# Performance work log

Hardware: AMD Instinct MI355X
Metric: run time of the kernel (lower is better)

Reference implementation:

```python
import jax, jax.numpy as jnp
import numpy as np

ALPHA = 0.2
N_ENT, N_TYP, N_REL, E = 100000, 1000, 200, 500000
D = 64          # nfeat1 = nfeat2 = nhid1 = nhid2 = relation_dim
NHEADS = 2      # forced by the tuple-unpack in the original forward


def _xavier(key, shape):
    fan_out, fan_in = shape[0], shape[-1]
    lim = 1.414 * np.sqrt(6.0 / (fan_in + fan_out))
    return jax.random.uniform(key, shape, jnp.float32, -lim, lim)


def setup_inputs() -> dict:
    key = jax.random.key(0)
    ks = jax.random.split(key, 32)
    inp = {
        "entity_embeddings": jax.random.normal(ks[0], (N_ENT, D), jnp.float32),
        "type_embed": jax.random.normal(ks[1], (N_TYP, D), jnp.float32),
        "relation_embed": jax.random.normal(ks[2], (N_REL, D), jnp.float32),
        "edge_list": jax.random.randint(ks[3], (2, E), 0, N_TYP),  # row0=src entity, row1=dst type; both in-range
        "edge_type": jax.random.randint(ks[4], (E,), 0, N_REL),
        "edge_embed": jax.random.normal(ks[5], (E, D), jnp.float32),
    }
    Din = 3 * D  # cat(x1[src], x2[dst], edge_embed)
    i = 6
    for h in range(NHEADS):
        inp[f"a_e{h}"] = _xavier(ks[i], (D, Din)); i += 1   # entity-side attention proj
        inp[f"v_e{h}"] = _xavier(ks[i], (1, D))[0]; i += 1  # entity-side score vector
        inp[f"a_t{h}"] = _xavier(ks[i], (D, Din)); i += 1   # type-side attention proj
        inp[f"v_t{h}"] = _xavier(ks[i], (1, D))[0]; i += 1
    Ho = NHEADS * D       # 128
    Dout = 3 * Ho         # out layer input cat dim
    inp["a_eo"] = _xavier(ks[i], (Ho, Dout)); i += 1
    inp["v_eo"] = _xavier(ks[i], (1, Ho))[0]; i += 1
    inp["a_to"] = _xavier(ks[i], (Ho, Dout)); i += 1
    inp["v_to"] = _xavier(ks[i], (1, Ho))[0]; i += 1
    inp["W"] = _xavier(ks[i], (D, Ho))  # relation_dim -> nheads*nhid1
    return inp


def _gat_e2t(x1, x2, src, dst, e, a_e, v_e, a_t, v_t, concat):
    """Bipartite sparse GAT layer (KBGAT-style, e2t variant).
    Message m = a @ cat(x1[src], x2[dst], edge_embed); score = exp(-leaky_relu(v . m));
    softmax-normalized scatter-aggregate to entity nodes (by src) and type nodes (by dst)."""
    d1, d2 = x1.shape[1], x2.shape[1]

    def agg(a, v, seg, nseg):
        a1, a2, a3 = a[:, :d1], a[:, d1:d1 + d2], a[:, d1 + d2:]
        # project nodes first, then gather (avoids materializing [E, 3d] cat)
        m = (x1 @ a1.T)[src] + (x2 @ a2.T)[dst] + e @ a3.T     # [E, h]
        s = jnp.exp(-jax.nn.leaky_relu(m @ v, ALPHA))          # [E] unnormalized attention
        num = jax.ops.segment_sum(m * s[:, None], seg, num_segments=nseg)
        den = jax.ops.segment_sum(s, seg, num_segments=nseg)
        h = num / jnp.where(den == 0, 1.0, den)[:, None]
        return jax.nn.elu(h) if concat else h

    h_e = agg(a_e, v_e, src, x1.shape[0])
    h_t = agg(a_t, v_t, dst, x2.shape[0])
    return h_e, h_t


def reference(entity_embeddings, type_embed, relation_embed, edge_list, edge_type, edge_embed,
              a_e0, v_e0, a_t0, v_t0, a_e1, v_e1, a_t1, v_t1,
              a_eo, v_eo, a_to, v_to, W):
    src, dst = edge_list[0], edge_list[1]
    # two attention heads (concat=True -> elu inside)
    h0e, h0t = _gat_e2t(entity_embeddings, type_embed, src, dst, edge_embed, a_e0, v_e0, a_t0, v_t0, True)
    h1e, h1t = _gat_e2t(entity_embeddings, type_embed, src, dst, edge_embed, a_e1, v_e1, a_t1, v_t1, True)
    x1 = jnp.concatenate([h0e, h1e], axis=1)  # [N_ENT, 2*nhid1]
    x2 = jnp.concatenate([h0t, h1t], axis=1)  # [N_TYP, 2*nhid2]
    # dropout is identity at inference
    out_rel = relation_embed @ W              # [N_REL, nheads*nhid1]
    e2 = out_rel[edge_type]                   # per-edge relation embedding
    o1, o2 = _gat_e2t(x1, x2, src, dst, e2, a_eo, v_eo, a_to, v_to, False)
    return jax.nn.elu(o1), jax.nn.elu(o2), out_rel
```

## Files before the change

kernel.cpp:

```cpp
#include <hip/hip_runtime.h>

#define ALPHA 0.2f
#define NT 1000
#define NRELC 200
#define NE 500000
#define N_ENT 100000
#define CH 2048
#define G 245

static constexpr size_t I_STARTS_SRC = 0;
static constexpr size_t I_STARTS_DST = 1001;
static constexpr size_t I_COLSUM     = 2002;
static constexpr size_t I_HIST2      = 4002;
static constexpr size_t I_BASE2      = 494002;
static constexpr size_t I_AB_SRC     = 984004;
static constexpr size_t I_AB_DST     = 2984004;

static constexpr size_t F_U1 = 4984004;
static constexpr size_t F_U2 = F_U1 + 768;
static constexpr size_t F_L1 = F_U2 + 768;
static constexpr size_t F_X1 = F_L1 + 4*130000;
static constexpr size_t F_X2 = F_X1 + 128000;
static constexpr size_t F_OR = F_X2 + 128000;
static constexpr size_t F_L2 = F_OR + 25600;
static constexpr size_t S2F = 283800;
static constexpr size_t WS_FLOATS = F_L2 + 2*S2F;

static constexpr size_t OUT_O2  = 12800000;
static constexpr size_t OUT_REL = 12928000;

__device__ __forceinline__ float eluf(float x) { return x > 0.f ? x : expm1f(x); }
__device__ __forceinline__ float scoref(float slin) {
  return expf(slin > 0.f ? -slin : -ALPHA * slin);
}

__global__ __launch_bounds__(256) void k_hist2(const int* __restrict__ src,
                                               const int* __restrict__ dst,
                                               int* __restrict__ ip) {
  __shared__ int h[NT];
  int bid = blockIdx.x;
  int side = bid >= G;
  int blk = bid - side * G;
  const int* keys = side ? dst : src;
  int j0 = blk * CH;
  int n = min(CH, NE - j0);
  for (int i = threadIdx.x; i < NT; i += 256) h[i] = 0;
  __syncthreads();
  for (int k = threadIdx.x; k < n; k += 256) atomicAdd(&h[keys[j0 + k]], 1);
  __syncthreads();
  int* row = ip + I_HIST2 + (size_t)(side * G + blk) * NT;
  for (int b = threadIdx.x; b < NT; b += 256) row[b] = h[b];
}

__global__ void k_colsum(int* __restrict__ ip) {
  int t = blockIdx.x * 256 + threadIdx.x;
  if (t >= 2 * NT) return;
  int side = t / NT, bin = t - side * NT;
  int s = 0;
  for (int blk = 0; blk < G; ++blk)
    s += ip[I_HIST2 + (size_t)(side * G + blk) * NT + bin];
  ip[I_COLSUM + t] = s;
}

__global__ void k_scan2b(int* __restrict__ ip) {
  __shared__ int buf[1024];
  int t = threadIdx.x;
  for (int side = 0; side < 2; ++side) {
    int v = (t < NT) ? ip[I_COLSUM + side * NT + t] : 0;
    buf[t] = v;
    __syncthreads();
    for (int off = 1; off < 1024; off <<= 1) {
      int x = (t >= off) ? buf[t - off] : 0;
      __syncthreads();
      buf[t] += x;
      __syncthreads();
    }
    int* st = ip + (side ? I_STARTS_DST : I_STARTS_SRC);
    if (t < NT) st[t] = buf[t] - v;
    if (t == NT - 1) st[NT] = buf[t];
    __syncthreads();
  }
}

__global__ void k_bases(int* __restrict__ ip) {
  int t = blockIdx.x * 256 + threadIdx.x;
  if (t >= 2 * NT) return;
  int side = t / NT, bin = t - side * NT;
  int run = ip[(side ? I_STARTS_DST : I_STARTS_SRC) + bin];
  for (int blk = 0; blk < G; ++blk) {
    size_t idx = I_HIST2 + (size_t)(side * G + blk) * NT + bin;
    int c = ip[idx];
    ip[idx + (I_BASE2 - I_HIST2)] = run;
    run += c;
  }
}

__global__ void k_prep_u(const float* aE0, const float* vE0, const float* aT0, const float* vT0,
                         const float* aE1, const float* vE1, const float* aT1, const float* vT1,
                         const float* aEo, const float* vEo, const float* aTo, const float* vTo,
                         float* ws) {
  int t = blockIdx.x * blockDim.x + threadIdx.x;
  if (t < 768) {
    int c = t / 192, rem = t - c*192;
    int p = rem >> 6, k = rem & 63;
    const float* a = (c==0)?aE0:(c==1)?aT0:(c==2)?aE1:aT1;
    const float* v = (c==0)?vE0:(c==1)?vT0:(c==2)?vE1:vT1;
    float s = 0.f;
    for (int o = 0; o < 64; ++o) s += a[o*192 + p*64 + k] * v[o];
    ws[F_U1 + (size_t)(c*3+p)*64 + k] = s;
  } else if (t < 1536) {
    int tt = t - 768;
    int c = tt / 384, rem = tt - c*384;
    int p = rem >> 7, k = rem & 127;
    const float* a = c ? aTo : aEo;
    const float* v = c ? vTo : vEo;
    float s = 0.f;
    for (int o = 0; o < 128; ++o) s += a[o*384 + p*128 + k] * v[o];
    ws[F_U2 + (size_t)(c*3+p)*128 + k] = s;
  }
}

__global__ __launch_bounds__(256) void k_l1_proj(const float* Ent, const float* Typ,
                                                 const float* aE0, const float* aT0,
                                                 const float* aE1, const float* aT1,
                                                 float* ws) {
  int bid = blockIdx.x;
  int t = threadIdx.x;
  if (bid < 504) {
    __shared__ float xs[16][64];
    int c = bid / 126, rem = bid - c*126;
    int table = rem / 63, tile = rem - table*63;
    int i0 = tile * 16;
    const float* a = (c==0)?aE0:(c==1)?aT0:(c==2)?aE1:aT1;
    const float* x = table ? Typ : Ent;
    float* outb = ws + F_L1 + (size_t)c*130000 + (table ? 64000 : 0);
    for (int idx = t; idx < 1024; idx += 256) {
      int r = idx >> 6, k = idx & 63;
      int i = i0 + r;
      xs[r][k] = (i < NT) ? x[(size_t)i*64 + k] : 0.f;
    }
    __syncthreads();
    int o = t & 63, grp = t >> 6;
    const float* arow = a + o*192 + table*64;
    float acc0 = 0.f, acc1 = 0.f, acc2 = 0.f, acc3 = 0.f;
    #pragma unroll 8
    for (int k = 0; k < 64; ++k) {
      float av = arow[k];
      acc0 += xs[grp*4+0][k] * av;
      acc1 += xs[grp*4+1][k] * av;
      acc2 += xs[grp*4+2][k] * av;
      acc3 += xs[grp*4+3][k] * av;
    }
    int ib = i0 + grp*4;
    if (ib + 0 < NT) outb[(size_t)(ib+0)*64 + o] = acc0;
    if (ib + 1 < NT) outb[(size_t)(ib+1)*64 + o] = acc1;
    if (ib + 2 < NT) outb[(size_t)(ib+2)*64 + o] = acc2;
    if (ib + 3 < NT) outb[(size_t)(ib+3)*64 + o] = acc3;
  } else {
    int idx = (bid - 504) * 256 + t;
    if (idx >= 8000) return;
    int c = idx / 2000, rem = idx - c*2000;
    float* base = ws + F_L1 + (size_t)c * 130000;
    if (rem < 1000) {
      const float* x = Ent + (size_t)rem*64;
      const float* u = ws + F_U1 + (size_t)(c*3)*64;
      float s = 0.f;
      #pragma unroll
      for (int k = 0; k < 64; ++k) s += x[k]*u[k];
      base[128000 + rem] = s;
    } else {
      int i = rem - 1000;
      const float* x = Typ + (size_t)i*64;
      const float* u = ws + F_U1 + (size_t)(c*3+1)*64;
      float s = 0.f;
      #pragma unroll
      for (int k = 0; k < 64; ++k) s += x[k]*u[k];
      base[129000 + i] = s;
    }
  }
}

__global__ __launch_bounds__(256) void k_binscat(const int* __restrict__ src,
                                                 const int* __restrict__ dst,
                                                 const int* __restrict__ et,
                                                 int* __restrict__ ip,
                                                 const float* __restrict__ ws) {
  __shared__ int2 bufs[CH];
  __shared__ int loff[1024];
  __shared__ int lcur[1024];
  __shared__ int gbase[1024];
  __shared__ int psum[256];
  int bid = blockIdx.x;
  int side = bid >= G;
  int blk = bid - side * G;
  const int* keys = side ? dst : src;
  const int* oths = side ? src : dst;
  int j0 = blk * CH;
  int n = min(CH, NE - j0);
  int t = threadIdx.x;

  for (int i = t; i < 1024; i += 256) lcur[i] = 0;
  __syncthreads();
  for (int k = t; k < n; k += 256) atomicAdd(&lcur[keys[j0 + k]], 1);
  __syncthreads();
  int c0 = lcur[4*t], c1 = lcur[4*t+1], c2 = lcur[4*t+2], c3 = lcur[4*t+3];
  int s = c0 + c1 + c2 + c3;
  psum[t] = s;
  __syncthreads();
  for (int off = 1; off < 256; off <<= 1) {
    int x = (t >= off) ? psum[t - off] : 0;
    __syncthreads();
    psum[t] += x;
    __syncthreads();
  }
  int base = psum[t] - s;
  loff[4*t]   = base;
  loff[4*t+1] = base + c0;
  loff[4*t+2] = base + c0 + c1;
  loff[4*t+3] = base + c0 + c1 + c2;
  lcur[4*t]   = loff[4*t];
  lcur[4*t+1] = loff[4*t+1];
  lcur[4*t+2] = loff[4*t+2];
  lcur[4*t+3] = loff[4*t+3];
  const int* brow = ip + I_BASE2 + (size_t)(side * G + blk) * NT;
  for (int b = t; b < NT; b += 256) gbase[b] = brow[b];
  __syncthreads();
  for (int k = t; k < n; k += 256) {
    int j = j0 + k;
    int b = keys[j];
    int pos = atomicAdd(&lcur[b], 1);
    bufs[pos] = make_int2(j | (b << 19), oths[j] | (et[j] << 16));
  }
  __syncthreads();
  size_t othOff = side ? 128000 : 129000;
  const float* cT0 = ws + F_L1 + (size_t)(side    )*130000 + othOff;
  const float* cT1 = ws + F_L1 + (size_t)(side + 2)*130000 + othOff;
  int4* out4 = reinterpret_cast<int4*>(ip + (side ? I_AB_DST : I_AB_SRC));
  for (int k = t; k < n; k += 256) {
    int2 q = bufs[k];
    int b = q.x >> 19;
    int posg = gbase[b] + (k - loff[b]);
    int oth = q.y & 0xFFFF;
    out4[posg] = make_int4(q.x & 0x7FFFF, q.y,
                           __float_as_int(cT0[oth]), __float_as_int(cT1[oth]));
  }
}

__global__ __launch_bounds__(256) void k_l1_acc(const float* __restrict__ Eemb,
                                                const float* aE0, const float* aT0,
                                                const float* aE1, const float* aT1,
                                                const int* __restrict__ ip,
                                                float* __restrict__ ws) {
  __shared__ float smem[3154];
  float* TlB   = smem;
  float* accRf = smem + 2000;
  float* accEf = smem + 3024;
  float* denf  = smem + 3152;
  float* redf  = smem + 2000;

  int side = blockIdx.x >= NT;
  int g = blockIdx.x - side * NT;
  int t = threadIdx.x;
  int sub = t & 15, slot = t >> 4;
  int c0 = side, c1 = side + 2;

  size_t ownOff = side ? 129000 : 128000;
  for (int i = t; i < NT; i += 256) { TlB[i] = 0.f; TlB[1000 + i] = 0.f; }
  if (t < 2) denf[t] = 0.f;
  float ownA = ws[F_L1 + (size_t)c0*130000 + ownOff + g];
  float ownB = ws[F_L1 + (size_t)c1*130000 + ownOff + g];
  float4 w3A = reinterpret_cast<const float4*>(ws + F_U1 + (size_t)(c0*3+2)*64)[sub];
  float4 w3B = reinterpret_cast<const float4*>(ws + F_U1 + (size_t)(c1*3+2)*64)[sub];
  __syncthreads();

  int start = ip[(side ? I_STARTS_DST : I_STARTS_SRC) + g];
  int end   = ip[(side ? I_STARTS_DST : I_STARTS_SRC) + g + 1];
  const int4* ab = reinterpret_cast<const int4*>(ip + (side ? I_AB_DST : I_AB_SRC));
  const float4* EV = reinterpret_cast<const float4*>(Eemb);

  float4 acc0 = make_float4(0.f,0.f,0.f,0.f);
  float4 acc1 = make_float4(0.f,0.f,0.f,0.f);
  float d0 = 0.f, d1 = 0.f;

  int p = start + slot;
  for (; p + 48 < end; p += 64) {
    int4 q0 = ab[p], q1 = ab[p+16], q2 = ab[p+32], q3 = ab[p+48];
    float4 e0 = EV[(size_t)q0.x*16 + sub];
    float4 e1 = EV[(size_t)q1.x*16 + sub];
    float4 e2 = EV[(size_t)q2.x*16 + sub];
    float4 e3 = EV[(size_t)q3.x*16 + sub];
    float rA0 = e0.x*w3A.x + e0.y*w3A.y + e0.z*w3A.z + e0.w*w3A.w;
    float rB0 = e0.x*w3B.x + e0.y*w3B.y + e0.z*w3B.z + e0.w*w3B.w;
    float rA1 = e1.x*w3A.x + e1.y*w3A.y + e1.z*w3A.z + e1.w*w3A.w;
    float rB1 = e1.x*w3B.x + e1.y*w3B.y + e1.z*w3B.z + e1.w*w3B.w;
    float rA2 = e2.x*w3A.x + e2.y*w3A.y + e2.z*w3A.z + e2.w*w3A.w;
    float rB2 = e2.x*w3B.x + e2.y*w3B.y + e2.z*w3B.z + e2.w*w3B.w;
    float rA3 = e3.x*w3A.x + e3.y*w3A.y + e3.z*w3A.z + e3.w*w3A.w;
    float rB3 = e3.x*w3B.x + e3.y*w3B.y + e3.z*w3B.z + e3.w*w3B.w;
    #pragma unroll
    for (int sh = 1; sh < 16; sh <<= 1) {
      rA0 += __shfl_xor(rA0, sh, 16); rB0 += __shfl_xor(rB0, sh, 16);
      rA1 += __shfl_xor(rA1, sh, 16); rB1 += __shfl_xor(rB1, sh, 16);
      rA2 += __shfl_xor(rA2, sh, 16); rB2 += __shfl_xor(rB2, sh, 16);
      rA3 += __shfl_xor(rA3, sh, 16); rB3 += __shfl_xor(rB3, sh, 16);
    }
    int o0 = q0.y & 0xFFFF, o1 = q1.y & 0xFFFF, o2 = q2.y & 0xFFFF, o3 = q3.y & 0xFFFF;
    float sA0 = scoref(ownA + __int_as_float(q0.z) + rA0);
    float sB0 = scoref(ownB + __int_as_float(q0.w) + rB0);
    float sA1 = scoref(ownA + __int_as_float(q1.z) + rA1);
    float sB1 = scoref(ownB + __int_as_float(q1.w) + rB1);
    float sA2 = scoref(ownA + __int_as_float(q2.z) + rA2);
    float sB2 = scoref(ownB + __int_as_float(q2.w) + rB2);
    float sA3 = scoref(ownA + __int_as_float(q3.z) + rA3);
    float sB3 = scoref(ownB + __int_as_float(q3.w) + rB3);
    acc0.x += sA0*e0.x + sA1*e1.x + sA2*e2.x + sA3*e3.x;
    acc0.y += sA0*e0.y + sA1*e1.y + sA2*e2.y + sA3*e3.y;
    acc0.z += sA0*e0.z + sA1*e1.z + sA2*e2.z + sA3*e3.z;
    acc0.w += sA0*e0.w + sA1*e1.w + sA2*e2.w + sA3*e3.w;
    acc1.x += sB0*e0.x + sB1*e1.x + sB2*e2.x + sB3*e3.x;
    acc1.y += sB0*e0.y + sB1*e1.y + sB2*e2.y + sB3*e3.y;
    acc1.z += sB0*e0.z + sB1*e1.z + sB2*e2.z + sB3*e3.z;
    acc1.w += sB0*e0.w + sB1*e1.w + sB2*e2.w + sB3*e3.w;
    if (sub == 0) {
      atomicAdd(&TlB[o0], sA0); atomicAdd(&TlB[1000+o0], sB0);
      atomicAdd(&TlB[o1], sA1); atomicAdd(&TlB[1000+o1], sB1);
      atomicAdd(&TlB[o2], sA2); atomicAdd(&TlB[1000+o2], sB2);
      atomicAdd(&TlB[o3], sA3); atomicAdd(&TlB[1000+o3], sB3);
      d0 += sA0 + sA1 + sA2 + sA3;
      d1 += sB0 + sB1 + sB2 + sB3;
    }
  }
  for (; p < end; p += 16) {
    int4 q = ab[p];
    float4 ev = EV[(size_t)q.x*16 + sub];
    float rA = ev.x*w3A.x + ev.y*w3A.y + ev.z*w3A.z + ev.w*w3A.w;
    float rB = ev.x*w3B.x + ev.y*w3B.y + ev.z*w3B.z + ev.w*w3B.w;
    #pragma unroll
    for (int sh = 1; sh < 16; sh <<= 1) {
      rA += __shfl_xor(rA, sh, 16);
      rB += __shfl_xor(rB, sh, 16);
    }
    int oth = q.y & 0xFFFF;
    float sA = scoref(ownA + __int_as_float(q.z) + rA);
    float sB = scoref(ownB + __int_as_float(q.w) + rB);
    acc0.x += sA*ev.x; acc0.y += sA*ev.y; acc0.z += sA*ev.z; acc0.w += sA*ev.w;
    acc1.x += sB*ev.x; acc1.y += sB*ev.y; acc1.z += sB*ev.z; acc1.w += sB*ev.w;
    if (sub == 0) {
      atomicAdd(&TlB[oth], sA);
      atomicAdd(&TlB[1000+oth], sB);
      d0 += sA; d1 += sB;
    }
  }
  if (sub == 0) { atomicAdd(&denf[0], d0); atomicAdd(&denf[1], d1); }
  __syncthreads();
  *reinterpret_cast<float4*>(&accRf[slot*64 + sub*4]) = acc0;
  __syncthreads();
  if (t < 64) {
    float s = 0.f;
    #pragma unroll
    for (int sl = 0; sl < 16; ++sl) s += accRf[sl*64 + t];
    accEf[t] = s;
  }
  __syncthreads();
  *reinterpret_cast<float4*>(&accRf[slot*64 + sub*4]) = acc1;
  __syncthreads();
  if (t < 64) {
    float s = 0.f;
    #pragma unroll
    for (int sl = 0; sl < 16; ++sl) s += accRf[sl*64 + t];
    accEf[64 + t] = s;
  }
  __syncthreads();

  int o = t & 63, part = t >> 6;
  size_t othPOff = side ? 0 : 64000;
  size_t ownPOff = side ? 64000 : 0;
  #pragma unroll
  for (int ci = 0; ci < 2; ++ci) {
    int c = side + 2*ci;
    const float* Pc = ws + F_L1 + (size_t)c * 130000;
    const float* Poth = Pc + othPOff;
    float sum = 0.f;
    for (int dd = part*250; dd < part*250 + 250; ++dd)
      sum += TlB[ci*1000 + dd] * Poth[(size_t)dd*64 + o];
    redf[t] = sum;
    __syncthreads();
    if (part == 0) {
      sum = redf[o] + redf[64+o] + redf[128+o] + redf[192+o];
      const float* a = (c==0)?aE0:(c==1)?aT0:(c==2)?aE1:aT1;
      const float* a3 = a + o*192 + 128;
      float acc = 0.f;
      #pragma unroll
      for (int k = 0; k < 64; ++k) acc += accEf[ci*64 + k]*a3[k];
      float den = denf[ci];
      float own = Pc[ownPOff + (size_t)g*64 + o];
      float num = sum + acc + den*own;
      float h = num / (den == 0.f ? 1.f : den);
      float* dst = ws + (side ? F_X2 : F_X1);
      dst[(size_t)g*128 + ci*64 + o] = eluf(h);
    }
    __syncthreads();
  }
}

__global__ void k_relW(const float* Rel, const float* W, float* ws, float* dout) {
  int t = blockIdx.x * blockDim.x + threadIdx.x;
  if (t >= NRELC*128) return;
  int r = t >> 7, o = t & 127;
  const float* x = Rel + (size_t)r*64;
  float s = 0.f;
  #pragma unroll
  for (int k = 0; k < 64; ++k) s += x[k] * W[(size_t)k*128 + o];
  ws[F_OR + t] = s;
  dout[OUT_REL + t] = s;
}

__global__ __launch_bounds__(256) void k_l2_proj(const float* aEo, const float* aTo,
                                                 float* ws) {
  int bid = blockIdx.x;
  int t = threadIdx.x;
  const float* x1 = ws + F_X1;
  const float* x2 = ws + F_X2;
  const float* orel = ws + F_OR;
  if (bid < 278) {
    __shared__ float xs[16][128];
    int c = bid / 139, rem = bid - c*139;
    const float* a = c ? aTo : aEo;
    float* cb = ws + F_L2 + (size_t)c * S2F;
    const float* x; int part, tile, nrows; float* outb;
    if (rem < 63)       { x = x1;   part = 0; tile = rem;       nrows = NT;    outb = cb; }
    else if (rem < 126) { x = x2;   part = 1; tile = rem - 63;  nrows = NT;    outb = cb + 128000; }
    else                { x = orel; part = 2; tile = rem - 126; nrows = NRELC; outb = cb + 256000; }
    int i0 = tile * 16;
    for (int idx = t; idx < 2048; idx += 256) {
      int r = idx >> 7, k = idx & 127;
      int i = i0 + r;
      xs[r][k] = (i < nrows) ? x[(size_t)i*128 + k] : 0.f;
    }
    __syncthreads();
    int o = t & 127, grp = t >> 7;
    const float* arow = a + (size_t)o*384 + part*128;
    float acc[8] = {0.f,0.f,0.f,0.f,0.f,0.f,0.f,0.f};
    #pragma unroll 4
    for (int k = 0; k < 128; ++k) {
      float av = arow[k];
      #pragma unroll
      for (int r = 0; r < 8; ++r)
        acc[r] += xs[grp*8+r][k] * av;
    }
    int ib = i0 + grp*8;
    #pragma unroll
    for (int r = 0; r < 8; ++r)
      if (ib + r < nrows) outb[(size_t)(ib+r)*128 + o] = acc[r];
  } else {
    int idx = (bid - 278) * 256 + t;
    if (idx >= 4400) return;
    int c = idx / 2200, rem = idx - c*2200;
    float* base = ws + F_L2 + (size_t)c * S2F;
    if (rem < 1000) {
      const float* u = ws + F_U2 + (size_t)(c*3)*128;
      const float* x = x1 + (size_t)rem*128;
      float s = 0.f;
      for (int k = 0; k < 128; ++k) s += x[k]*u[k];
      base[281600 + rem] = s;
    } else if (rem < 2000) {
      int i = rem - 1000;
      const float* u = ws + F_U2 + (size_t)(c*3+1)*128;
      const float* x = x2 + (size_t)i*128;
      float s = 0.f;
      for (int k = 0; k < 128; ++k) s += x[k]*u[k];
      base[282600 + i] = s;
    } else {
      int r = rem - 2000;
      const float* u = ws + F_U2 + (size_t)(c*3+2)*128;
      const float* x = orel + (size_t)r*128;
      float s = 0.f;
      for (int k = 0; k < 128; ++k) s += x[k]*u[k];
      base[283600 + r] = s;
    }
  }
}

__global__ __launch_bounds__(256) void k_l2_seg(const int* __restrict__ ip,
                                                float* __restrict__ ws,
                                                float* __restrict__ dout) {
  __shared__ float Tl[2][NT];
  __shared__ float Ul[2][NRELC];
  __shared__ float cOthL[NT];
  __shared__ float cRelL[NRELC];
  __shared__ float red[2][256];
  __shared__ float denl[2];

  int c = blockIdx.x >= 500;
  int gp = blockIdx.x - c * 500;
  int g0 = gp * 2;
  int t = threadIdx.x;
  float* base = ws + F_L2 + (size_t)c * S2F;

  size_t othOff = c ? 281600 : 282600;
  size_t ownOff = c ? 282600 : 281600;
  for (int i = t; i < NT; i += 256) { Tl[0][i] = 0.f; Tl[1][i] = 0.f; cOthL[i] = base[othOff + i]; }
  for (int i = t; i < NRELC; i += 256) { Ul[0][i] = 0.f; Ul[1][i] = 0.f; cRelL[i] = base[283600 + i]; }
  if (t < 2) denl[t] = 0.f;
  float own0 = base[ownOff + g0];
  float own1 = base[ownOff + g0 + 1];
  __syncthreads();

  const int* st = ip + (c ? I_STARTS_DST : I_STARTS_SRC);
  int s0 = st[g0], split = st[g0 + 1], e1 = st[g0 + 2];
  const int4* ab = reinterpret_cast<const int4*>(ip + (c ? I_AB_DST : I_AB_SRC));

  float d0 = 0.f, d1 = 0.f;
  for (int p = s0 + t; p < e1; p += 256) {
    int4 q = ab[p];
    int oth = q.y & 0xFFFF;
    int r = q.y >> 16;
    int ls = p >= split;
    float sv = scoref((ls ? own1 : own0) + cOthL[oth] + cRelL[r]);
    atomicAdd(&Tl[ls][oth], sv);
    atomicAdd(&Ul[ls][r], sv);
    if (ls) d1 += sv; else d0 += sv;
  }
  atomicAdd(&denl[0], d0);
  atomicAdd(&denl[1], d1);
  __syncthreads();

  int o = t & 127, part = t >> 7;
  const float* Qoth = base + (c ? 0 : 128000);
  const float* R3 = base + 256000;
  float sum0 = 0.f, sum1 = 0.f;
  for (int dd = part*500; dd < part*500 + 500; ++dd) {
    float qv = Qoth[(size_t)dd*128 + o];
    sum0 += Tl[0][dd] * qv;
    sum1 += Tl[1][dd] * qv;
  }
  for (int rr = part*100; rr < part*100 + 100; ++rr) {
    float qv = R3[(size_t)rr*128 + o];
    sum0 += Ul[0][rr] * qv;
    sum1 += Ul[1][rr] * qv;
  }
  red[0][t] = sum0;
  red[1][t] = sum1;
  __syncthreads();
  int li = part;
  float den = denl[li];
  float sum = red[li][o] + red[li][128 + o];
  int gw = g0 + li;
  float ownQ = base[(c ? 128000 : 0) + (size_t)gw*128 + o];
  float num = sum + den * ownQ;
  float h = num / (den == 0.f ? 1.f : den);
  size_t off = c ? (OUT_O2 + (size_t)gw*128 + o) : ((size_t)gw*128 + o);
  dout[off] = eluf(h);
}

extern "C" void kernel_launch(void* const* d_in, const int* in_sizes, int n_in,
                              void* d_out, int out_size, void* d_ws, size_t ws_size,
                              hipStream_t stream) {
  (void)in_sizes; (void)n_in;
  const float* Ent = (const float*)d_in[0];
  const float* Typ = (const float*)d_in[1];
  const float* Rel = (const float*)d_in[2];
  const int*   edge = (const int*)d_in[3];
  const int*   etyp = (const int*)d_in[4];
  const float* Eemb = (const float*)d_in[5];
  const float* aE0 = (const float*)d_in[6];
  const float* vE0 = (const float*)d_in[7];
  const float* aT0 = (const float*)d_in[8];
  const float* vT0 = (const float*)d_in[9];
  const float* aE1 = (const float*)d_in[10];
  const float* vE1 = (const float*)d_in[11];
  const float* aT1 = (const float*)d_in[12];
  const float* vT1 = (const float*)d_in[13];
  const float* aEo = (const float*)d_in[14];
  const float* vEo = (const float*)d_in[15];
  const float* aTo = (const float*)d_in[16];
  const float* vTo = (const float*)d_in[17];
  const float* W   = (const float*)d_in[18];
  float* ws  = (float*)d_ws;
  int*   ip  = (int*)d_ws;
  float* out = (float*)d_out;
  const int* srcA = edge;
  const int* dstA = edge + NE;

  if (ws_size < WS_FLOATS * sizeof(float)) return;

  hipMemsetAsync(d_out, 0, (size_t)out_size * sizeof(float), stream);

  k_hist2  <<<2*G, 256, 0, stream>>>(srcA, dstA, ip);
  k_colsum <<<8, 256, 0, stream>>>(ip);
  k_scan2b <<<1, 1024, 0, stream>>>(ip);
  k_bases  <<<8, 256, 0, stream>>>(ip);
  k_prep_u <<<6, 256, 0, stream>>>(aE0,vE0,aT0,vT0,aE1,vE1,aT1,vT1,aEo,vEo,aTo,vTo,ws);
  k_l1_proj<<<536, 256, 0, stream>>>(Ent, Typ, aE0, aT0, aE1, aT1, ws);
  k_binscat<<<2*G, 256, 0, stream>>>(srcA, dstA, etyp, ip, ws);
  k_l1_acc <<<2000, 256, 0, stream>>>(Eemb, aE0, aT0, aE1, aT1, ip, ws);
  k_relW   <<<100, 256, 0, stream>>>(Rel, W, ws, out);
  k_l2_proj<<<296, 256, 0, stream>>>(aEo, aTo, ws);
  k_l2_seg <<<1000, 256, 0, stream>>>(ip, ws, out);
}
```

Baseline: 256.3 us.

## Precompute per-edge layer-1 attention scores once before binning

Adds a kernel that computes, for every edge, the edge-embedding dot products with all four layer-1 score vectors in one coalesced pass. The binning kernel then computes the final exp-leaky-relu scores and stores them in the packed edge records. The accumulation kernel no longer needs the per-edge dot products and shuffle reductions, which were previously done twice (once per side) with gathered loads. In exchange it adds a full streaming read of the edge embeddings, an 8 MB workspace buffer and an extra kernel launch.

```diff
diff --git a/kernel.cpp b/kernel.cpp
--- a/kernel.cpp
+++ b/kernel.cpp
@@ -24,7 +24,8 @@
 static constexpr size_t F_OR = F_X2 + 128000;
 static constexpr size_t F_L2 = F_OR + 25600;
 static constexpr size_t S2F = 283800;
-static constexpr size_t WS_FLOATS = F_L2 + 2*S2F;
+static constexpr size_t F_R4 = F_L2 + 2*S2F;
+static constexpr size_t WS_FLOATS = F_R4 + 2000000;
 
 static constexpr size_t OUT_O2  = 12800000;
 static constexpr size_t OUT_REL = 12928000;
@@ -180,6 +181,32 @@
   }
 }
 
+__global__ __launch_bounds__(256) void k_rdots(const float* __restrict__ Eemb,
+                                               float* __restrict__ ws) {
+  int t = blockIdx.x * 256 + threadIdx.x;
+  int j = t >> 4, sub = t & 15;
+  if (j >= NE) return;
+  float4 ev = reinterpret_cast<const float4*>(Eemb)[t];
+  const float4* U = reinterpret_cast<const float4*>(ws + F_U1);
+  float4 w0 = U[ 2*16 + sub];
+  float4 w1 = U[ 5*16 + sub];
+  float4 w2 = U[ 8*16 + sub];
+  float4 w3 = U[11*16 + sub];
+  float r0 = ev.x*w0.x + ev.y*w0.y + ev.z*w0.z + ev.w*w0.w;
+  float r1 = ev.x*w1.x + ev.y*w1.y + ev.z*w1.z + ev.w*w1.w;
+  float r2 = ev.x*w2.x + ev.y*w2.y + ev.z*w2.z + ev.w*w2.w;
+  float r3 = ev.x*w3.x + ev.y*w3.y + ev.z*w3.z + ev.w*w3.w;
+  #pragma unroll
+  for (int s = 1; s < 16; s <<= 1) {
+    r0 += __shfl_xor(r0, s, 16);
+    r1 += __shfl_xor(r1, s, 16);
+    r2 += __shfl_xor(r2, s, 16);
+    r3 += __shfl_xor(r3, s, 16);
+  }
+  if (sub == 0)
+    reinterpret_cast<float4*>(ws + F_R4)[j] = make_float4(r0, r1, r2, r3);
+}
+
 __global__ __launch_bounds__(256) void k_binscat(const int* __restrict__ src,
                                                  const int* __restrict__ dst,
                                                  const int* __restrict__ et,
@@ -232,17 +259,26 @@
     bufs[pos] = make_int2(j | (b << 19), oths[j] | (et[j] << 16));
   }
   __syncthreads();
+  size_t ownOff = side ? 129000 : 128000;
   size_t othOff = side ? 128000 : 129000;
-  const float* cT0 = ws + F_L1 + (size_t)(side    )*130000 + othOff;
-  const float* cT1 = ws + F_L1 + (size_t)(side + 2)*130000 + othOff;
+  const float* ownA = ws + F_L1 + (size_t)(side    )*130000 + ownOff;
+  const float* ownB = ws + F_L1 + (size_t)(side + 2)*130000 + ownOff;
+  const float* othA = ws + F_L1 + (size_t)(side    )*130000 + othOff;
+  const float* othB = ws + F_L1 + (size_t)(side + 2)*130000 + othOff;
+  const float4* R4 = reinterpret_cast<const float4*>(ws + F_R4);
   int4* out4 = reinterpret_cast<int4*>(ip + (side ? I_AB_DST : I_AB_SRC));
   for (int k = t; k < n; k += 256) {
     int2 q = bufs[k];
     int b = q.x >> 19;
     int posg = gbase[b] + (k - loff[b]);
+    int j = q.x & 0x7FFFF;
     int oth = q.y & 0xFFFF;
-    out4[posg] = make_int4(q.x & 0x7FFFF, q.y,
-                           __float_as_int(cT0[oth]), __float_as_int(cT1[oth]));
+    float4 r = R4[j];
+    float rA = side ? r.y : r.x;
+    float rB = side ? r.w : r.z;
+    float sA = scoref(ownA[b] + othA[oth] + rA);
+    float sB = scoref(ownB[b] + othB[oth] + rB);
+    out4[posg] = make_int4(j, q.y, __float_as_int(sA), __float_as_int(sB));
   }
 }
 
@@ -262,15 +298,9 @@
   int g = blockIdx.x - side * NT;
   int t = threadIdx.x;
   int sub = t & 15, slot = t >> 4;
-  int c0 = side, c1 = side + 2;
-
-  size_t ownOff = side ? 129000 : 128000;
+
   for (int i = t; i < NT; i += 256) { TlB[i] = 0.f; TlB[1000 + i] = 0.f; }
   if (t < 2) denf[t] = 0.f;
-  float ownA = ws[F_L1 + (size_t)c0*130000 + ownOff + g];
-  float ownB = ws[F_L1 + (size_t)c1*130000 + ownOff + g];
-  float4 w3A = reinterpret_cast<const float4*>(ws + F_U1 + (size_t)(c0*3+2)*64)[sub];
-  float4 w3B = reinterpret_cast<const float4*>(ws + F_U1 + (size_t)(c1*3+2)*64)[sub];
   __syncthreads();
 
   int start = ip[(side ? I_STARTS_DST : I_STARTS_SRC) + g];
@@ -289,30 +319,10 @@
     float4 e1 = EV[(size_t)q1.x*16 + sub];
     float4 e2 = EV[(size_t)q2.x*16 + sub];
     float4 e3 = EV[(size_t)q3.x*16 + sub];
-    float rA0 = e0.x*w3A.x + e0.y*w3A.y + e0.z*w3A.z + e0.w*w3A.w;
-    float rB0 = e0.x*w3B.x + e0.y*w3B.y + e0.z*w3B.z + e0.w*w3B.w;
-    float rA1 = e1.x*w3A.x + e1.y*w3A.y + e1.z*w3A.z + e1.w*w3A.w;
-    float rB1 = e1.x*w3B.x + e1.y*w3B.y + e1.z*w3B.z + e1.w*w3B.w;
-    float rA2 = e2.x*w3A.x + e2.y*w3A.y + e2.z*w3A.z + e2.w*w3A.w;
-    float rB2 = e2.x*w3B.x + e2.y*w3B.y + e2.z*w3B.z + e2.w*w3B.w;
-    float rA3 = e3.x*w3A.x + e3.y*w3A.y + e3.z*w3A.z + e3.w*w3A.w;
-    float rB3 = e3.x*w3B.x + e3.y*w3B.y + e3.z*w3B.z + e3.w*w3B.w;
-    #pragma unroll
-    for (int sh = 1; sh < 16; sh <<= 1) {
-      rA0 += __shfl_xor(rA0, sh, 16); rB0 += __shfl_xor(rB0, sh, 16);
-      rA1 += __shfl_xor(rA1, sh, 16); rB1 += __shfl_xor(rB1, sh, 16);
-      rA2 += __shfl_xor(rA2, sh, 16); rB2 += __shfl_xor(rB2, sh, 16);
-      rA3 += __shfl_xor(rA3, sh, 16); rB3 += __shfl_xor(rB3, sh, 16);
-    }
-    int o0 = q0.y & 0xFFFF, o1 = q1.y & 0xFFFF, o2 = q2.y & 0xFFFF, o3 = q3.y & 0xFFFF;
-    float sA0 = scoref(ownA + __int_as_float(q0.z) + rA0);
-    float sB0 = scoref(ownB + __int_as_float(q0.w) + rB0);
-    float sA1 = scoref(ownA + __int_as_float(q1.z) + rA1);
-    float sB1 = scoref(ownB + __int_as_float(q1.w) + rB1);
-    float sA2 = scoref(ownA + __int_as_float(q2.z) + rA2);
-    float sB2 = scoref(ownB + __int_as_float(q2.w) + rB2);
-    float sA3 = scoref(ownA + __int_as_float(q3.z) + rA3);
-    float sB3 = scoref(ownB + __int_as_float(q3.w) + rB3);
+    float sA0 = __int_as_float(q0.z), sB0 = __int_as_float(q0.w);
+    float sA1 = __int_as_float(q1.z), sB1 = __int_as_float(q1.w);
+    float sA2 = __int_as_float(q2.z), sB2 = __int_as_float(q2.w);
+    float sA3 = __int_as_float(q3.z), sB3 = __int_as_float(q3.w);
     acc0.x += sA0*e0.x + sA1*e1.x + sA2*e2.x + sA3*e3.x;
     acc0.y += sA0*e0.y + sA1*e1.y + sA2*e2.y + sA3*e3.y;
     acc0.z += sA0*e0.z + sA1*e1.z + sA2*e2.z + sA3*e3.z;
@@ -322,6 +332,7 @@
     acc1.z += sB0*e0.z + sB1*e1.z + sB2*e2.z + sB3*e3.z;
     acc1.w += sB0*e0.w + sB1*e1.w + sB2*e2.w + sB3*e3.w;
     if (sub == 0) {
+      int o0 = q0.y & 0xFFFF, o1 = q1.y & 0xFFFF, o2 = q2.y & 0xFFFF, o3 = q3.y & 0xFFFF;
       atomicAdd(&TlB[o0], sA0); atomicAdd(&TlB[1000+o0], sB0);
       atomicAdd(&TlB[o1], sA1); atomicAdd(&TlB[1000+o1], sB1);
       atomicAdd(&TlB[o2], sA2); atomicAdd(&TlB[1000+o2], sB2);
@@ -333,19 +344,11 @@
   for (; p < end; p += 16) {
     int4 q = ab[p];
     float4 ev = EV[(size_t)q.x*16 + sub];
-    float rA = ev.x*w3A.x + ev.y*w3A.y + ev.z*w3A.z + ev.w*w3A.w;
-    float rB = ev.x*w3B.x + ev.y*w3B.y + ev.z*w3B.z + ev.w*w3B.w;
-    #pragma unroll
-    for (int sh = 1; sh < 16; sh <<= 1) {
-      rA += __shfl_xor(rA, sh, 16);
-      rB += __shfl_xor(rB, sh, 16);
-    }
-    int oth = q.y & 0xFFFF;
-    float sA = scoref(ownA + __int_as_float(q.z) + rA);
-    float sB = scoref(ownB + __int_as_float(q.w) + rB);
+    float sA = __int_as_float(q.z), sB = __int_as_float(q.w);
     acc0.x += sA*ev.x; acc0.y += sA*ev.y; acc0.z += sA*ev.z; acc0.w += sA*ev.w;
     acc1.x += sB*ev.x; acc1.y += sB*ev.y; acc1.z += sB*ev.z; acc1.w += sB*ev.w;
     if (sub == 0) {
+      int oth = q.y & 0xFFFF;
       atomicAdd(&TlB[oth], sA);
       atomicAdd(&TlB[1000+oth], sB);
       d0 += sA; d1 += sB;
@@ -592,6 +595,7 @@
   k_bases  <<<8, 256, 0, stream>>>(ip);
   k_prep_u <<<6, 256, 0, stream>>>(aE0,vE0,aT0,vT0,aE1,vE1,aT1,vT1,aEo,vEo,aTo,vTo,ws);
   k_l1_proj<<<536, 256, 0, stream>>>(Ent, Typ, aE0, aT0, aE1, aT1, ws);
+  k_rdots  <<<31250, 256, 0, stream>>>(Eemb, ws);
   k_binscat<<<2*G, 256, 0, stream>>>(srcA, dstA, etyp, ip, ws);
   k_l1_acc <<<2000, 256, 0, stream>>>(Eemb, aE0, aT0, aE1, aT1, ip, ws);
   k_relW   <<<100, 256, 0, stream>>>(Rel, W, ws, out);
```

Result: slower. 273.0 us (+6.5%).
